# Kernel tuning notes

Hardware: AMD Instinct MI355X
Metric: run time of the kernel (lower is better)

## Reference

```python
import jax, jax.numpy as jnp
import numpy as np

TEMP = 0.07
DIAG_FILL = -10.0


def setup_inputs() -> dict:
    key = jax.random.key(0)
    k1, k2 = jax.random.split(key)
    N, D = 8192, 256
    feat_q = jax.random.normal(k1, (N, D), dtype=jnp.float32)
    feat_k = jax.random.normal(k2, (N, D), dtype=jnp.float32)
    return {"feat_q": feat_q, "feat_k": feat_k}


def reference(feat_q, feat_k):
    # feat_k is detached in the original module
    feat_k = jax.lax.stop_gradient(feat_k)
    N = feat_q.shape[0]

    q_norm = jnp.linalg.norm(feat_q, axis=-1, keepdims=True)  # [N,1]
    k_norm = jnp.linalg.norm(feat_k, axis=-1, keepdims=True)  # [N,1]

    # positive logits: cosine similarity of matching patches -> [N,1]
    l_pos = jnp.sum(feat_q * feat_k, axis=-1, keepdims=True) / (q_norm * k_norm)

    # negative logits: pairwise cosine similarities -> [N,N]
    l_neg = jnp.einsum('nd,md->nm', feat_q, feat_k) / (q_norm * k_norm.T)
    # mask diagonal (self pairs) with -10.0
    diag = jnp.eye(N, dtype=bool)
    l_neg = jnp.where(diag, jnp.float32(DIAG_FILL), l_neg)

    out = jnp.concatenate([l_pos, l_neg], axis=1) / TEMP  # [N, 1+N]
    # cross-entropy with target class 0, reduction='none'
    loss = jax.nn.logsumexp(out, axis=1) - out[:, 0]
    return loss
```

## Files before the change

kernel.cpp:

```cpp
#include <hip/hip_runtime.h>
#include <stdint.h>

#define N_ROWS 8192
#define DIM 256

constexpr float INV_T = 1.0f / 0.07f;
constexpr float M0    = 1.0f / 0.07f;
constexpr float LOG2E = 1.44269504088896f;
constexpr float C1    = INV_T * LOG2E;
constexpr float C0    = -M0 * LOG2E;
constexpr float KSCL  = 127.0f / 0.35f;

typedef int i32x4  __attribute__((ext_vector_type(4)));
typedef int i32x16 __attribute__((ext_vector_type(16)));

__device__ inline float fast_exp2(float x) {
    float r;
    asm("v_exp_f32 %0, %1" : "=v"(r) : "v"(x));
    return r;
}
__device__ inline int pack4(int a, int b, int c, int d) {
    return (a & 0xff) | ((b & 0xff) << 8) | ((c & 0xff) << 16) | (d << 24);
}

__global__ __launch_bounds__(256) void prep_kernel(
    const float* __restrict__ q, const float* __restrict__ k,
    int* __restrict__ qi8, int* __restrict__ ki8,
    float* __restrict__ lposT, float* __restrict__ fqs) {
    const int wid  = threadIdx.x >> 6;
    const int lane = threadIdx.x & 63;
    const int row  = blockIdx.x * 4 + wid;

    const float4 qv = *reinterpret_cast<const float4*>(q + (size_t)row * DIM + lane * 4);
    const float4 kv = *reinterpret_cast<const float4*>(k + (size_t)row * DIM + lane * 4);

    float qq = qv.x*qv.x + qv.y*qv.y + qv.z*qv.z + qv.w*qv.w;
    float kk = kv.x*kv.x + kv.y*kv.y + kv.z*kv.z + kv.w*kv.w;
    float qk = qv.x*kv.x + qv.y*kv.y + qv.z*kv.z + qv.w*kv.w;
    float qm = fmaxf(fmaxf(fabsf(qv.x), fabsf(qv.y)), fmaxf(fabsf(qv.z), fabsf(qv.w)));

    #pragma unroll
    for (int off = 32; off > 0; off >>= 1) {
        qq += __shfl_xor(qq, off, 64);
        kk += __shfl_xor(kk, off, 64);
        qk += __shfl_xor(qk, off, 64);
        qm  = fmaxf(qm, __shfl_xor(qm, off, 64));
    }
    const float iq = 1.0f / sqrtf(qq);
    const float ik = 1.0f / sqrtf(kk);

    const float ksc = ik * KSCL;
    int k0 = __float2int_rn(fminf(fmaxf(kv.x * ksc, -127.f), 127.f));
    int k1 = __float2int_rn(fminf(fmaxf(kv.y * ksc, -127.f), 127.f));
    int k2 = __float2int_rn(fminf(fmaxf(kv.z * ksc, -127.f), 127.f));
    int k3 = __float2int_rn(fminf(fmaxf(kv.w * ksc, -127.f), 127.f));
    ki8[(size_t)row * 64 + lane] = pack4(k0, k1, k2, k3);

    const float qsc = 127.0f / qm;
    int q0 = __float2int_rn(qv.x * qsc);
    int q1 = __float2int_rn(qv.y * qsc);
    int q2 = __float2int_rn(qv.z * qsc);
    int q3 = __float2int_rn(qv.w * qsc);
    qi8[(size_t)row * 64 + lane] = pack4(q0, q1, q2, q3);

    if (lane == 0) {
        lposT[row] = qk * iq * ik * INV_T;
        fqs[row] = C1 * (0.35f / (127.0f * 127.0f)) * qm * iq;
    }
}

__global__ __launch_bounds__(256, 2) void gemm_lse_kernel(
    const uint8_t* __restrict__ qi8, const uint8_t* __restrict__ ki8,
    const float* __restrict__ fqs, float* __restrict__ ps) {
    __shared__ char lds[2 * 16384];
    char* const B0 = lds;
    char* const B1 = lds + 16384;

    const int tid  = threadIdx.x;
    const int lane = tid & 63;
    const int wid  = tid >> 6;
    const int l31  = lane & 31;
    const int l5   = lane >> 5;

    const int qtile = blockIdx.x;
    const int strip = blockIdx.y;
    const int qw    = qtile * 256 + wid * 64;
    const int ks0   = strip * 512;

    auto stage = [&](int t, char* dst) {
        const int kr0 = ks0 + t * 64;
        #pragma unroll
        for (int s = 0; s < 4; ++s) {
            const int n    = wid * 4 + s;
            const int lrow = n * 8 + (lane >> 3);
            const int row  = lrow & 63;
            const int kh   = lrow >> 6;
            const uint8_t* gp = ki8 + (size_t)(kr0 + row) * 256 + kh * 128
                              + (((lane & 7) ^ (lrow & 7)) << 4);
            __builtin_amdgcn_global_load_lds(
                (const __attribute__((address_space(1))) void*)gp,
                (__attribute__((address_space(3))) void*)(dst + n * 1024),
                16, 0, 0);
        }
    };

    stage(0, B0);

    i32x4 qf[8][2];
    #pragma unroll
    for (int ks = 0; ks < 8; ++ks)
        #pragma unroll
        for (int cg = 0; cg < 2; ++cg)
            qf[ks][cg] = *reinterpret_cast<const i32x4*>(
                qi8 + (size_t)(qw + cg * 32 + l31) * 256 + ks * 32 + l5 * 16);

    const float f0 = fqs[qw + l31];
    const float f1 = fqs[qw + 32 + l31];

    asm volatile("s_waitcnt vmcnt(0)" ::: "memory");
    __builtin_amdgcn_s_barrier();

    i32x16 acc00 = {}, acc01 = {}, acc10 = {}, acc11 = {};
    float ssum0 = 0.f, ssum1 = 0.f;

    auto lda = [&](const char* src, int rg, i32x4* a) {
        const int row = rg * 32 + l31;
        #pragma unroll
        for (int ks = 0; ks < 8; ++ks) {
            const int o    = ks * 32 + l5 * 16;
            const int lrow = row + ((o >> 7) << 6);
            const int slot = ((o & 127) >> 4) ^ (lrow & 7);
            a[ks] = *reinterpret_cast<const i32x4*>(src + lrow * 128 + (slot << 4));
        }
    };

    auto expfrag = [&](i32x16& A, bool diag, float f, float& ss) {
        float s = 0.f;
        #pragma unroll
        for (int r = 0; r < 16; ++r) {
            float e = fast_exp2(fmaf((float)A[r], f, C0));
            if (diag && (((r & 3) + 8 * (r >> 2) + 4 * l5) == l31)) e = 0.f;
            s += e;
            A[r] = 0;
        }
        ss += s;
    };

    #pragma unroll 1
    for (int t = 0; t < 8; ++t) {
        char* const cur = (t & 1) ? B1 : B0;
        char* const nxt = (t & 1) ? B0 : B1;
        if (t < 7) {
            stage(t + 1, nxt);
            asm volatile("s_waitcnt vmcnt(4)" ::: "memory");
        } else {
            asm volatile("s_waitcnt vmcnt(0)" ::: "memory");
        }
        __builtin_amdgcn_s_barrier();
        __builtin_amdgcn_sched_barrier(0);

        const int kc0 = ks0 + t * 64;
        i32x4 a0[8], a1[8];
        lda(cur, 0, a0);
        __builtin_amdgcn_s_setprio(1);
        #pragma unroll
        for (int ks = 0; ks < 8; ++ks) {
            acc00 = __builtin_amdgcn_mfma_i32_32x32x32_i8(a0[ks], qf[ks][0], acc00, 0, 0, 0);
            acc01 = __builtin_amdgcn_mfma_i32_32x32x32_i8(a0[ks], qf[ks][1], acc01, 0, 0, 0);
        }
        __builtin_amdgcn_s_setprio(0);
        lda(cur, 1, a1);
        __builtin_amdgcn_s_setprio(1);
        #pragma unroll
        for (int ks = 0; ks < 8; ++ks) {
            acc10 = __builtin_amdgcn_mfma_i32_32x32x32_i8(a1[ks], qf[ks][0], acc10, 0, 0, 0);
            acc11 = __builtin_amdgcn_mfma_i32_32x32x32_i8(a1[ks], qf[ks][1], acc11, 0, 0, 0);
        }
        __builtin_amdgcn_s_setprio(0);

        expfrag(acc00, kc0      == qw,      f0, ssum0);
        expfrag(acc01, kc0      == qw + 32, f1, ssum1);
        expfrag(acc10, kc0 + 32 == qw,      f0, ssum0);
        expfrag(acc11, kc0 + 32 == qw + 32, f1, ssum1);

        __builtin_amdgcn_s_barrier();
    }

    ssum0 += __shfl_xor(ssum0, 32, 64);
    ssum1 += __shfl_xor(ssum1, 32, 64);
    if (lane < 32) {
        ps[(size_t)(qw + l31) * 16 + strip]      = ssum0;
        ps[(size_t)(qw + 32 + l31) * 16 + strip] = ssum1;
    }
}

__global__ __launch_bounds__(256) void finalize_kernel(
    const float* __restrict__ ps, const float* __restrict__ lposT,
    float* __restrict__ out) {
    const int row = blockIdx.x * 256 + threadIdx.x;
    float S = 0.f;
    #pragma unroll
    for (int c = 0; c < 4; ++c) {
        const float4 p = *reinterpret_cast<const float4*>(ps + (size_t)row * 16 + c * 4);
        S += p.x + p.y + p.z + p.w;
    }
    const float lp = lposT[row];
    S += __expf(lp - M0);
    out[row] = M0 + logf(S) - lp;
}

extern "C" void kernel_launch(void* const* d_in, const int* in_sizes, int n_in,
                              void* d_out, int out_size, void* d_ws, size_t ws_size,
                              hipStream_t stream) {
    const float* q = (const float*)d_in[0];
    const float* k = (const float*)d_in[1];
    float* out = (float*)d_out;

    char* ws = (char*)d_ws;
    int*   qi8 = (int*)(ws);
    int*   ki8 = (int*)(ws + (2u << 20));
    float* lpt = (float*)(ws + (4u << 20));
    float* fqs = (float*)(ws + (4u << 20) + (32u << 10));
    float* ps  = (float*)(ws + (4u << 20) + (64u << 10));

    prep_kernel<<<N_ROWS / 4, 256, 0, stream>>>(q, k, qi8, ki8, lpt, fqs);
    dim3 grid(32, 16);
    gemm_lse_kernel<<<grid, 256, 0, stream>>>((const uint8_t*)qi8, (const uint8_t*)ki8, fqs, ps);
    finalize_kernel<<<N_ROWS / 256, 256, 0, stream>>>(ps, lpt, out);
}
```

Measured before the change: 37.37 us.

## Split key tile across warp pairs and overlap exp of previous tile with loads

Each block now covers 128 query rows instead of 256. Warps are paired so each warp handles one 32-row half of the key tile for a 64-query group, which halves the accumulators per warp. The grid doubles and the launch bound is raised to allow three blocks per CU. The exp/sum of the previous tile's accumulators is deferred into the next iteration, so it overlaps the in-flight global-to-LDS staging. The partial-sum buffer doubles to 32 entries per row and finalize reads twice as much. In exchange, each K tile is loaded by twice as many blocks, raising LDS and global traffic.

```diff
diff --git a/kernel.cpp b/kernel.cpp
--- a/kernel.cpp
+++ b/kernel.cpp
@@ -69,7 +69,7 @@
     }
 }
 
-__global__ __launch_bounds__(256, 2) void gemm_lse_kernel(
+__global__ __launch_bounds__(256, 3) void gemm_lse_kernel(
     const uint8_t* __restrict__ qi8, const uint8_t* __restrict__ ki8,
     const float* __restrict__ fqs, float* __restrict__ ps) {
     __shared__ char lds[2 * 16384];
@@ -84,7 +84,9 @@
 
     const int qtile = blockIdx.x;
     const int strip = blockIdx.y;
-    const int qw    = qtile * 256 + wid * 64;
+    const int rg    = wid & 1;
+    const int cw    = wid >> 1;
+    const int qw    = qtile * 128 + cw * 64;
     const int ks0   = strip * 512;
 
     auto stage = [&](int t, char* dst) {
@@ -120,10 +122,10 @@
     asm volatile("s_waitcnt vmcnt(0)" ::: "memory");
     __builtin_amdgcn_s_barrier();
 
-    i32x16 acc00 = {}, acc01 = {}, acc10 = {}, acc11 = {};
+    i32x16 acc0 = {}, acc1 = {};
     float ssum0 = 0.f, ssum1 = 0.f;
 
-    auto lda = [&](const char* src, int rg, i32x4* a) {
+    auto lda = [&](const char* src, i32x4* a) {
         const int row = rg * 32 + l31;
         #pragma unroll
         for (int ks = 0; ks < 8; ++ks) {
@@ -150,47 +152,41 @@
     for (int t = 0; t < 8; ++t) {
         char* const cur = (t & 1) ? B1 : B0;
         char* const nxt = (t & 1) ? B0 : B1;
-        if (t < 7) {
-            stage(t + 1, nxt);
-            asm volatile("s_waitcnt vmcnt(4)" ::: "memory");
-        } else {
-            asm volatile("s_waitcnt vmcnt(0)" ::: "memory");
-        }
+        if (t < 7) stage(t + 1, nxt);
+
+        if (t > 0) {
+            const int kp = ks0 + (t - 1) * 64 + rg * 32;
+            expfrag(acc0, kp == qw,      f0, ssum0);
+            expfrag(acc1, kp == qw + 32, f1, ssum1);
+        }
+
+        if (t < 7) { asm volatile("s_waitcnt vmcnt(4)" ::: "memory"); }
+        else       { asm volatile("s_waitcnt vmcnt(0)" ::: "memory"); }
         __builtin_amdgcn_s_barrier();
         __builtin_amdgcn_sched_barrier(0);
 
-        const int kc0 = ks0 + t * 64;
-        i32x4 a0[8], a1[8];
-        lda(cur, 0, a0);
+        i32x4 a[8];
+        lda(cur, a);
         __builtin_amdgcn_s_setprio(1);
         #pragma unroll
         for (int ks = 0; ks < 8; ++ks) {
-            acc00 = __builtin_amdgcn_mfma_i32_32x32x32_i8(a0[ks], qf[ks][0], acc00, 0, 0, 0);
-            acc01 = __builtin_amdgcn_mfma_i32_32x32x32_i8(a0[ks], qf[ks][1], acc01, 0, 0, 0);
+            acc0 = __builtin_amdgcn_mfma_i32_32x32x32_i8(a[ks], qf[ks][0], acc0, 0, 0, 0);
+            acc1 = __builtin_amdgcn_mfma_i32_32x32x32_i8(a[ks], qf[ks][1], acc1, 0, 0, 0);
         }
         __builtin_amdgcn_s_setprio(0);
-        lda(cur, 1, a1);
-        __builtin_amdgcn_s_setprio(1);
-        #pragma unroll
-        for (int ks = 0; ks < 8; ++ks) {
-            acc10 = __builtin_amdgcn_mfma_i32_32x32x32_i8(a1[ks], qf[ks][0], acc10, 0, 0, 0);
-            acc11 = __builtin_amdgcn_mfma_i32_32x32x32_i8(a1[ks], qf[ks][1], acc11, 0, 0, 0);
-        }
-        __builtin_amdgcn_s_setprio(0);
-
-        expfrag(acc00, kc0      == qw,      f0, ssum0);
-        expfrag(acc01, kc0      == qw + 32, f1, ssum1);
-        expfrag(acc10, kc0 + 32 == qw,      f0, ssum0);
-        expfrag(acc11, kc0 + 32 == qw + 32, f1, ssum1);
-
         __builtin_amdgcn_s_barrier();
+    }
+    {
+        const int kp = ks0 + 7 * 64 + rg * 32;
+        expfrag(acc0, kp == qw,      f0, ssum0);
+        expfrag(acc1, kp == qw + 32, f1, ssum1);
     }
 
     ssum0 += __shfl_xor(ssum0, 32, 64);
     ssum1 += __shfl_xor(ssum1, 32, 64);
     if (lane < 32) {
-        ps[(size_t)(qw + l31) * 16 + strip]      = ssum0;
-        ps[(size_t)(qw + 32 + l31) * 16 + strip] = ssum1;
+        ps[(size_t)(qw + l31) * 32 + strip * 2 + rg]      = ssum0;
+        ps[(size_t)(qw + 32 + l31) * 32 + strip * 2 + rg] = ssum1;
     }
 }
 
@@ -200,8 +196,8 @@
     const int row = blockIdx.x * 256 + threadIdx.x;
     float S = 0.f;
     #pragma unroll
-    for (int c = 0; c < 4; ++c) {
-        const float4 p = *reinterpret_cast<const float4*>(ps + (size_t)row * 16 + c * 4);
+    for (int c = 0; c < 8; ++c) {
+        const float4 p = *reinterpret_cast<const float4*>(ps + (size_t)row * 32 + c * 4);
         S += p.x + p.y + p.z + p.w;
     }
     const float lp = lposT[row];
@@ -224,7 +220,7 @@
     float* ps  = (float*)(ws + (4u << 20) + (64u << 10));
 
     prep_kernel<<<N_ROWS / 4, 256, 0, stream>>>(q, k, qi8, ki8, lpt, fqs);
-    dim3 grid(32, 16);
+    dim3 grid(64, 16);
     gemm_lse_kernel<<<grid, 256, 0, stream>>>((const uint8_t*)qi8, (const uint8_t*)ki8, fqs, ps);
     finalize_kernel<<<N_ROWS / 256, 256, 0, stream>>>(ps, lpt, out);
 }
```

Result: slower. 42.36 us (+13.3%).

## Triple-buffer K tiles in LDS and defer the exp epilogue by one tile

Applied to the files above, without the earlier changes.

The LDS staging of K tiles moves from a double buffer to a three-slot ring with two tiles prefetched ahead. This removes the second per-iteration barrier and the startup full wait. The exp/sum epilogue for tile t-1 now runs at the start of iteration t, and the loop is fully unrolled so the compiler can interleave it with the LDS reads for tile t. Diagonal checks that can never fire are constant-folded away. LDS use per block grows from 32 KB to 48 KB, which may reduce occupancy headroom.

```diff
diff --git a/kernel.cpp b/kernel.cpp
--- a/kernel.cpp
+++ b/kernel.cpp
@@ -72,9 +72,7 @@
 __global__ __launch_bounds__(256, 2) void gemm_lse_kernel(
     const uint8_t* __restrict__ qi8, const uint8_t* __restrict__ ki8,
     const float* __restrict__ fqs, float* __restrict__ ps) {
-    __shared__ char lds[2 * 16384];
-    char* const B0 = lds;
-    char* const B1 = lds + 16384;
+    __shared__ char lds[3 * 16384];
 
     const int tid  = threadIdx.x;
     const int lane = tid & 63;
@@ -87,7 +85,8 @@
     const int qw    = qtile * 256 + wid * 64;
     const int ks0   = strip * 512;
 
-    auto stage = [&](int t, char* dst) {
+    auto stage = [&](int t) {
+        char* dst = lds + (t % 3) * 16384;
         const int kr0 = ks0 + t * 64;
         #pragma unroll
         for (int s = 0; s < 4; ++s) {
@@ -104,8 +103,6 @@
         }
     };
 
-    stage(0, B0);
-
     i32x4 qf[8][2];
     #pragma unroll
     for (int ks = 0; ks < 8; ++ks)
@@ -113,12 +110,11 @@
         for (int cg = 0; cg < 2; ++cg)
             qf[ks][cg] = *reinterpret_cast<const i32x4*>(
                 qi8 + (size_t)(qw + cg * 32 + l31) * 256 + ks * 32 + l5 * 16);
-
     const float f0 = fqs[qw + l31];
     const float f1 = fqs[qw + 32 + l31];
 
-    asm volatile("s_waitcnt vmcnt(0)" ::: "memory");
-    __builtin_amdgcn_s_barrier();
+    stage(0);
+    stage(1);
 
     i32x16 acc00 = {}, acc01 = {}, acc10 = {}, acc11 = {};
     float ssum0 = 0.f, ssum1 = 0.f;
@@ -146,20 +142,24 @@
         ss += s;
     };
 
-    #pragma unroll 1
+    auto epilogue = [&](int t) {
+        const int kc0 = ks0 + t * 64;
+        expfrag(acc00, kc0 == qw, f0, ssum0);
+        expfrag(acc01, false,     f1, ssum1);
+        expfrag(acc10, false,     f0, ssum0);
+        expfrag(acc11, kc0 == qw, f1, ssum1);
+    };
+
+    #pragma unroll
     for (int t = 0; t < 8; ++t) {
-        char* const cur = (t & 1) ? B1 : B0;
-        char* const nxt = (t & 1) ? B0 : B1;
-        if (t < 7) {
-            stage(t + 1, nxt);
-            asm volatile("s_waitcnt vmcnt(4)" ::: "memory");
-        } else {
-            asm volatile("s_waitcnt vmcnt(0)" ::: "memory");
-        }
+        if (t < 7) { asm volatile("s_waitcnt vmcnt(4)" ::: "memory"); }
+        else       { asm volatile("s_waitcnt vmcnt(0)" ::: "memory"); }
         __builtin_amdgcn_s_barrier();
         __builtin_amdgcn_sched_barrier(0);
-
-        const int kc0 = ks0 + t * 64;
+        if (t < 6) stage(t + 2);
+        if (t > 0) epilogue(t - 1);
+
+        const char* cur = lds + (t % 3) * 16384;
         i32x4 a0[8], a1[8];
         lda(cur, 0, a0);
         __builtin_amdgcn_s_setprio(1);
@@ -177,14 +177,8 @@
             acc11 = __builtin_amdgcn_mfma_i32_32x32x32_i8(a1[ks], qf[ks][1], acc11, 0, 0, 0);
         }
         __builtin_amdgcn_s_setprio(0);
-
-        expfrag(acc00, kc0      == qw,      f0, ssum0);
-        expfrag(acc01, kc0      == qw + 32, f1, ssum1);
-        expfrag(acc10, kc0 + 32 == qw,      f0, ssum0);
-        expfrag(acc11, kc0 + 32 == qw + 32, f1, ssum1);
-
-        __builtin_amdgcn_s_barrier();
-    }
+    }
+    epilogue(7);
 
     ssum0 += __shfl_xor(ssum0, 32, 64);
     ssum1 += __shfl_xor(ssum1, 32, 64);
```

After: 36.91 us, median of 3. Within noise of the previous version (-1.2%).
